# Kernel tuning notes

Hardware: AMD Instinct MI355X
Metric: run time of the kernel (lower is better)

## Reference

```python
import jax, jax.numpy as jnp
import numpy as np

B, T, D_MODEL, N_HEAD = 2, 2048, 1024, 16
HEAD_DIM = D_MODEL // N_HEAD


def setup_inputs() -> dict:
    key = jax.random.key(0)
    ks = jax.random.split(key, 4)
    s = 0.02
    return {
        "x": jax.random.normal(ks[0], (B, T, D_MODEL), dtype=jnp.float32),
        "freqs_cis": jnp.zeros((T, HEAD_DIM // 2), dtype=jnp.float32),  # unused under ALiBi
        "Wq": jax.random.normal(ks[1], (D_MODEL, D_MODEL), dtype=jnp.float32) * s,
        "bq": jnp.zeros((D_MODEL,), dtype=jnp.float32),
        "Wkv": jax.random.normal(ks[2], (2 * D_MODEL, D_MODEL), dtype=jnp.float32) * s,
        "bkv": jnp.zeros((2 * D_MODEL,), dtype=jnp.float32),
        "Wo": jax.random.normal(ks[3], (D_MODEL, D_MODEL), dtype=jnp.float32) * s,
        "bo": jnp.zeros((D_MODEL,), dtype=jnp.float32),
    }


def reference(x, freqs_cis, Wq, bq, Wkv, bkv, Wo, bo):
    Bb, Tt, C = x.shape
    H, Dh = N_HEAD, HEAD_DIM
    # projections (torch Linear: x @ W^T + b)
    q = (x @ Wq.T + bq).reshape(Bb, Tt, H, Dh).transpose(0, 2, 1, 3)      # [B,H,T,Dh]
    kv = (x @ Wkv.T + bkv).reshape(Bb, Tt, 2, H, Dh).transpose(2, 0, 3, 1, 4)
    k, v = kv[0], kv[1]                                                    # [B,H,T,Dh]
    scores = jnp.einsum('bhqd,bhkd->bhqk', q, k) * (1.0 / np.sqrt(Dh))
    # ALiBi: linear slopes (1/H ... 1.0), bias = slope * (j - i)
    slopes = jnp.arange(1, H + 1, dtype=jnp.float32) / H                   # [H]
    pos = jnp.arange(Tt, dtype=jnp.float32)
    dist = pos[None, :] - pos[:, None]                                     # [T,T], j - i
    scores = scores + slopes[:, None, None] * dist[None]                   # broadcast over B
    # causal mask (upper triangle -> -inf)
    causal = pos[:, None] >= pos[None, :]                                  # [T,T] keep-mask
    scores = jnp.where(causal[None, None], scores, -jnp.inf)
    attn = jax.nn.softmax(scores, axis=-1)
    y = jnp.einsum('bhqk,bhkd->bhqd', attn, v)                             # [B,H,T,Dh]
    y = y.transpose(0, 2, 1, 3).reshape(Bb, Tt, C)
    return y @ Wo.T + bo
```

## Files before the change

### kernel.cpp

```cpp
#include <hip/hip_runtime.h>

typedef unsigned short u16;
typedef __bf16 bf16x8 __attribute__((ext_vector_type(8)));
typedef unsigned short u16x8 __attribute__((ext_vector_type(8)));
typedef float f32x4 __attribute__((ext_vector_type(4)));

#define KEY(r) ((((r) ^ ((r) >> 3)) & 7) << 3)

static __device__ __forceinline__ u16 f2b(float f) {
  union { float f; unsigned u; } x; x.f = f;
  unsigned r = x.u + 0x7FFFu + ((x.u >> 16) & 1u);
  return (u16)(r >> 16);
}

static __device__ __forceinline__ bf16x8 ld_frag(const u16* p) {
  union { u16x8 s; bf16x8 b; } u;
  u.s = *reinterpret_cast<const u16x8*>(p);
  return u.b;
}

__global__ __launch_bounds__(256) void cvt_f32_bf16(const float* __restrict__ in,
                                                    u16* __restrict__ out, int n4) {
  int i = blockIdx.x * 256 + threadIdx.x;
  if (i >= n4) return;
  float4 v = reinterpret_cast<const float4*>(in)[i];
  ushort4 o;
  o.x = f2b(v.x); o.y = f2b(v.y); o.z = f2b(v.z); o.w = f2b(v.w);
  reinterpret_cast<ushort4*>(out)[i] = o;
}

template <bool OUT_BF16>
static __device__ __forceinline__ void gemm_body(
    const u16* __restrict__ A, const u16* __restrict__ Bt,
    const float* __restrict__ bias, void* __restrict__ outp,
    int N, int K, int row0, int col0, float scale) {
  __shared__ alignas(16) u16 As[128 * 64];
  __shared__ alignas(16) u16 Bs[128 * 64];
  const int tid = threadIdx.x, wid = tid >> 6, lane = tid & 63;
  const int wr = wid >> 1, wc = wid & 1;
  const int lr = lane >> 3;
  const int lc = (lane & 7) * 8;
  const int frow = lane & 15, fk = (lane >> 4) * 8;
  f32x4 acc[4][4] = {};

  for (int k0 = 0; k0 < K; k0 += 64) {
    __syncthreads();
#pragma unroll
    for (int t = 0; t < 4; ++t) {
      const int r = wid * 32 + t * 8 + lr;
      __builtin_amdgcn_global_load_lds(
          (const __attribute__((address_space(1))) unsigned int*)(
              A + (size_t)(row0 + r) * K + k0 + (lc ^ KEY(r))),
          (__attribute__((address_space(3))) unsigned int*)(As + (wid * 32 + t * 8) * 64),
          16, 0, 0);
    }
#pragma unroll
    for (int t = 0; t < 4; ++t) {
      const int r = wid * 32 + t * 8 + lr;
      __builtin_amdgcn_global_load_lds(
          (const __attribute__((address_space(1))) unsigned int*)(
              Bt + (size_t)(col0 + r) * K + k0 + (lc ^ KEY(r))),
          (__attribute__((address_space(3))) unsigned int*)(Bs + (wid * 32 + t * 8) * 64),
          16, 0, 0);
    }
    __syncthreads();
#pragma unroll
    for (int ks = 0; ks < 2; ++ks) {
      bf16x8 a[4], b[4];
#pragma unroll
      for (int m = 0; m < 4; ++m) {
        const int r = wr * 64 + m * 16 + frow;
        a[m] = ld_frag(&As[r * 64 + ((ks * 32 + fk) ^ KEY(r))]);
      }
#pragma unroll
      for (int n = 0; n < 4; ++n) {
        const int r = wc * 64 + n * 16 + frow;
        b[n] = ld_frag(&Bs[r * 64 + ((ks * 32 + fk) ^ KEY(r))]);
      }
#pragma unroll
      for (int m = 0; m < 4; ++m)
#pragma unroll
        for (int n = 0; n < 4; ++n)
          acc[m][n] = __builtin_amdgcn_mfma_f32_16x16x32_bf16(a[m], b[n], acc[m][n], 0, 0, 0);
    }
  }
  const int colL = lane & 15, rb = (lane >> 4) * 4;
#pragma unroll
  for (int n = 0; n < 4; ++n) {
    const int gc = col0 + wc * 64 + n * 16 + colL;
    const float bv = bias[gc];
#pragma unroll
    for (int m = 0; m < 4; ++m)
#pragma unroll
      for (int r = 0; r < 4; ++r) {
        const int gr = row0 + wr * 64 + m * 16 + rb + r;
        const float v = (acc[m][n][r] + bv) * scale;
        if constexpr (OUT_BF16)
          reinterpret_cast<u16*>(outp)[(size_t)gr * N + gc] = f2b(v);
        else
          reinterpret_cast<float*>(outp)[(size_t)gr * N + gc] = v;
      }
  }
}

__global__ __launch_bounds__(256) void gemm_qkv(
    const u16* __restrict__ xb, const u16* __restrict__ wqb,
    const u16* __restrict__ wkvb, const float* __restrict__ bq,
    const float* __restrict__ bkv, u16* __restrict__ qb, u16* __restrict__ kvb) {
  const int row0 = blockIdx.x * 128;
  const int by = blockIdx.y;
  const u16* Bt; const float* bias; u16* out; int N, col0; float scale;
  if (by < 8) { Bt = wqb;  bias = bq;  out = qb;  N = 1024; col0 = by * 128;      scale = 0.125f; }
  else        { Bt = wkvb; bias = bkv; out = kvb; N = 2048; col0 = (by - 8) * 128; scale = 1.0f; }
  gemm_body<true>(xb, Bt, bias, out, N, 1024, row0, col0, scale);
}

__global__ __launch_bounds__(256) void gemm_o(
    const u16* __restrict__ yb, const u16* __restrict__ wob,
    const float* __restrict__ bo, float* __restrict__ out) {
  gemm_body<false>(yb, wob, bo, out, 1024, 1024, blockIdx.x * 128, blockIdx.y * 128, 1.0f);
}

__global__ __launch_bounds__(128) void attn_kernel(
    const u16* __restrict__ qb,
    const u16* __restrict__ kvb,
    u16* __restrict__ yb,
    int T) {
  const int C = 1024;
  const int bh = blockIdx.x;
  const int qt = gridDim.y - 1 - blockIdx.y;
  const int b = bh >> 4, h = bh & 15;
  const float slope = (float)(h + 1) * 0.0625f;
  const int tid = threadIdx.x, wid = tid >> 6, lane = tid & 63;
  const int qBase = qt * 32;

  __shared__ alignas(16) u16 Ks[64 * 64];
  __shared__ alignas(16) u16 Vt[64 * 64];
  __shared__ alignas(16) u16 Ps[2][16 * 64];

  const int frow = lane & 15, fk = (lane >> 4) * 8;
  const int col = lane & 15, rb = (lane >> 4) * 4;
  const int pk = ((lane >> 4) & 3) << 3;

  const int q_row = qBase + wid * 16 + frow;
  const u16* qp = qb + (size_t)(b * T + q_row) * C + h * 64;
  const bf16x8 aq0 = ld_frag(qp + fk);
  const bf16x8 aq1 = ld_frag(qp + 32 + fk);

  float mrow[4] = {-1e30f, -1e30f, -1e30f, -1e30f};
  float lrow[4] = {0.f, 0.f, 0.f, 0.f};
  f32x4 accO[4] = {};

  const int st_r = tid >> 3;
  const int st_c = (tid & 7) * 8;
  const int vkj = tid & 7;

  const int nt = (qBase + 31) / 64 + 1;

  int4 kreg[4], vreg[4];
#pragma unroll
  for (int t = 0; t < 4; ++t) {
    const int r = st_r + 16 * t;
    const size_t g = (size_t)(b * T + r) * 2048 + h * 64 + st_c;
    kreg[t] = *reinterpret_cast<const int4*>(&kvb[g]);
    vreg[t] = *reinterpret_cast<const int4*>(&kvb[g + 1024]);
  }

  for (int kt = 0; kt < nt; ++kt) {
    const int kBase = kt * 64;
#pragma unroll
    for (int t = 0; t < 4; ++t) {
      const int r = st_r + 16 * t;
      *reinterpret_cast<int4*>(&Ks[r * 64 + (st_c ^ KEY(r))]) = kreg[t];
      const u16* pv = reinterpret_cast<const u16*>(&vreg[t]);
#pragma unroll
      for (int j = 0; j < 8; ++j) {
        const int d = st_c + j;
        Vt[d * 64 + (r ^ ((((j) ^ vkj) & 7) << 3))] = pv[j];
      }
    }
    __syncthreads();
    if (kt + 1 < nt) {
#pragma unroll
      for (int t = 0; t < 4; ++t) {
        const int r = st_r + 16 * t;
        const size_t g = (size_t)(b * T + kBase + 64 + r) * 2048 + h * 64 + st_c;
        kreg[t] = *reinterpret_cast<const int4*>(&kvb[g]);
        vreg[t] = *reinterpret_cast<const int4*>(&kvb[g + 1024]);
      }
    }

    f32x4 accS[4] = {};
    __builtin_amdgcn_s_setprio(1);
#pragma unroll
    for (int n = 0; n < 4; ++n) {
      const int r = n * 16 + frow;
      bf16x8 bk0 = ld_frag(&Ks[r * 64 + (fk ^ KEY(r))]);
      accS[n] = __builtin_amdgcn_mfma_f32_16x16x32_bf16(aq0, bk0, accS[n], 0, 0, 0);
      bf16x8 bk1 = ld_frag(&Ks[r * 64 + ((32 + fk) ^ KEY(r))]);
      accS[n] = __builtin_amdgcn_mfma_f32_16x16x32_bf16(aq1, bk1, accS[n], 0, 0, 0);
    }
    __builtin_amdgcn_s_setprio(0);

    float bn[4]; int kg[4];
#pragma unroll
    for (int n = 0; n < 4; ++n) { kg[n] = kBase + n * 16 + col; bn[n] = slope * (float)kg[n]; }
#pragma unroll
    for (int r = 0; r < 4; ++r) {
      const int qg = qBase + wid * 16 + rb + r;
      float s[4];
      float tmax = -1e30f;
#pragma unroll
      for (int n = 0; n < 4; ++n) {
        float v = accS[n][r] + bn[n];
        if (kg[n] > qg) v = -1e30f;
        s[n] = v;
        tmax = fmaxf(tmax, v);
      }
      tmax = fmaxf(tmax, __shfl_xor(tmax, 1));
      tmax = fmaxf(tmax, __shfl_xor(tmax, 2));
      tmax = fmaxf(tmax, __shfl_xor(tmax, 4));
      tmax = fmaxf(tmax, __shfl_xor(tmax, 8));
      const float newm = fmaxf(mrow[r], tmax);
      const float corr = __expf(mrow[r] - newm);
      mrow[r] = newm;
      float psum = 0.f;
#pragma unroll
      for (int n = 0; n < 4; ++n) {
        const float p = __expf(s[n] - newm);
        psum += p;
        Ps[wid][(rb + r) * 64 + ((n * 16 + col) ^ pk)] = f2b(p);
      }
      psum += __shfl_xor(psum, 1);
      psum += __shfl_xor(psum, 2);
      psum += __shfl_xor(psum, 4);
      psum += __shfl_xor(psum, 8);
      lrow[r] = lrow[r] * corr + psum;
#pragma unroll
      for (int n = 0; n < 4; ++n) accO[n][r] *= corr;
    }

    __builtin_amdgcn_s_setprio(1);
#pragma unroll
    for (int ks = 0; ks < 2; ++ks) {
      const int pkr = ((frow >> 2) & 3) << 3;
      bf16x8 ap = ld_frag(&Ps[wid][frow * 64 + ((ks * 32 + fk) ^ pkr)]);
#pragma unroll
      for (int n = 0; n < 4; ++n) {
        const int d = n * 16 + frow;
        bf16x8 bv = ld_frag(&Vt[d * 64 + ((ks * 32 + fk) ^ KEY(d))]);
        accO[n] = __builtin_amdgcn_mfma_f32_16x16x32_bf16(ap, bv, accO[n], 0, 0, 0);
      }
    }
    __builtin_amdgcn_s_setprio(0);
    __syncthreads();
  }

#pragma unroll
  for (int r = 0; r < 4; ++r) {
    const float inv = 1.0f / lrow[r];
    const int qg = qBase + wid * 16 + rb + r;
    u16* yrow = yb + (size_t)(b * T + qg) * C + h * 64;
#pragma unroll
    for (int n = 0; n < 4; ++n) yrow[n * 16 + col] = f2b(accO[n][r] * inv);
  }
}

extern "C" void kernel_launch(void* const* d_in, const int* in_sizes, int n_in,
                              void* d_out, int out_size, void* d_ws, size_t ws_size,
                              hipStream_t stream) {
  const float* x   = (const float*)d_in[0];
  const float* Wq  = (const float*)d_in[2];
  const float* bq  = (const float*)d_in[3];
  const float* Wkv = (const float*)d_in[4];
  const float* bkv = (const float*)d_in[5];
  const float* Wo  = (const float*)d_in[6];
  const float* bo  = (const float*)d_in[7];
  float* out = (float*)d_out;

  const int B = 2, T = 2048, C = 1024;
  const int M = B * T;

  char* ws = (char*)d_ws;
  u16* xb   = (u16*)(ws + 0);
  u16* wqb  = (u16*)(ws + 8388608);
  u16* wkvb = (u16*)(ws + 10485760);
  u16* wob  = (u16*)(ws + 14680064);
  u16* qb   = (u16*)(ws + 16777216);
  u16* kvb  = (u16*)(ws + 25165824);
  u16* yb   = (u16*)(ws + 41943040);

  cvt_f32_bf16<<<(M * C / 4 + 255) / 256, 256, 0, stream>>>(x, xb, M * C / 4);
  cvt_f32_bf16<<<(C * C / 4 + 255) / 256, 256, 0, stream>>>(Wq, wqb, C * C / 4);
  cvt_f32_bf16<<<(2 * C * C / 4 + 255) / 256, 256, 0, stream>>>(Wkv, wkvb, 2 * C * C / 4);
  cvt_f32_bf16<<<(C * C / 4 + 255) / 256, 256, 0, stream>>>(Wo, wob, C * C / 4);

  gemm_qkv<<<dim3(M / 128, 8 + 16), 256, 0, stream>>>(xb, wqb, wkvb, bq, bkv, qb, kvb);
  attn_kernel<<<dim3(B * 16, T / 32), 128, 0, stream>>>(qb, kvb, yb, T);
  gemm_o<<<dim3(M / 128, C / 128), 256, 0, stream>>>(yb, wob, bo, out);
}
```

Baseline: 259.4 us.

## Enlarge attention query tile to 128 rows and narrow output GEMM tile

The attention kernel now processes 128 query rows per block with 4 waves, each handling two 16-row fragments. Each K/V tile loaded into LDS is therefore reused across four times more queries, which cuts redundant K/V global traffic and staging work. The output projection GEMM is templated on its N tile and uses 64-column tiles, doubling its grid for better occupancy on the CU count. The trade-off is fewer attention blocks, coarser causal granularity (some fully masked tiles get computed), and more registers per wave.

```diff
diff --git a/kernel.cpp b/kernel.cpp
--- a/kernel.cpp
+++ b/kernel.cpp
@@ -29,19 +29,20 @@
   reinterpret_cast<ushort4*>(out)[i] = o;
 }
 
-template <bool OUT_BF16>
+template <bool OUT_BF16, int BN>
 static __device__ __forceinline__ void gemm_body(
     const u16* __restrict__ A, const u16* __restrict__ Bt,
     const float* __restrict__ bias, void* __restrict__ outp,
     int N, int K, int row0, int col0, float scale) {
+  constexpr int NF = BN / 32;
   __shared__ alignas(16) u16 As[128 * 64];
-  __shared__ alignas(16) u16 Bs[128 * 64];
+  __shared__ alignas(16) u16 Bs[BN * 64];
   const int tid = threadIdx.x, wid = tid >> 6, lane = tid & 63;
   const int wr = wid >> 1, wc = wid & 1;
   const int lr = lane >> 3;
   const int lc = (lane & 7) * 8;
   const int frow = lane & 15, fk = (lane >> 4) * 8;
-  f32x4 acc[4][4] = {};
+  f32x4 acc[4][NF] = {};
 
   for (int k0 = 0; k0 < K; k0 += 64) {
     __syncthreads();
@@ -55,39 +56,39 @@
           16, 0, 0);
     }
 #pragma unroll
-    for (int t = 0; t < 4; ++t) {
-      const int r = wid * 32 + t * 8 + lr;
+    for (int t = 0; t < NF; ++t) {
+      const int r = wid * (BN / 4) + t * 8 + lr;
       __builtin_amdgcn_global_load_lds(
           (const __attribute__((address_space(1))) unsigned int*)(
               Bt + (size_t)(col0 + r) * K + k0 + (lc ^ KEY(r))),
-          (__attribute__((address_space(3))) unsigned int*)(Bs + (wid * 32 + t * 8) * 64),
+          (__attribute__((address_space(3))) unsigned int*)(Bs + (wid * (BN / 4) + t * 8) * 64),
           16, 0, 0);
     }
     __syncthreads();
 #pragma unroll
     for (int ks = 0; ks < 2; ++ks) {
-      bf16x8 a[4], b[4];
+      bf16x8 a[4], b[NF];
 #pragma unroll
       for (int m = 0; m < 4; ++m) {
         const int r = wr * 64 + m * 16 + frow;
         a[m] = ld_frag(&As[r * 64 + ((ks * 32 + fk) ^ KEY(r))]);
       }
 #pragma unroll
-      for (int n = 0; n < 4; ++n) {
-        const int r = wc * 64 + n * 16 + frow;
+      for (int n = 0; n < NF; ++n) {
+        const int r = wc * (BN / 2) + n * 16 + frow;
         b[n] = ld_frag(&Bs[r * 64 + ((ks * 32 + fk) ^ KEY(r))]);
       }
 #pragma unroll
       for (int m = 0; m < 4; ++m)
 #pragma unroll
-        for (int n = 0; n < 4; ++n)
+        for (int n = 0; n < NF; ++n)
           acc[m][n] = __builtin_amdgcn_mfma_f32_16x16x32_bf16(a[m], b[n], acc[m][n], 0, 0, 0);
     }
   }
   const int colL = lane & 15, rb = (lane >> 4) * 4;
 #pragma unroll
-  for (int n = 0; n < 4; ++n) {
-    const int gc = col0 + wc * 64 + n * 16 + colL;
+  for (int n = 0; n < NF; ++n) {
+    const int gc = col0 + wc * (BN / 2) + n * 16 + colL;
     const float bv = bias[gc];
 #pragma unroll
     for (int m = 0; m < 4; ++m)
@@ -112,16 +113,16 @@
   const u16* Bt; const float* bias; u16* out; int N, col0; float scale;
   if (by < 8) { Bt = wqb;  bias = bq;  out = qb;  N = 1024; col0 = by * 128;      scale = 0.125f; }
   else        { Bt = wkvb; bias = bkv; out = kvb; N = 2048; col0 = (by - 8) * 128; scale = 1.0f; }
-  gemm_body<true>(xb, Bt, bias, out, N, 1024, row0, col0, scale);
+  gemm_body<true, 128>(xb, Bt, bias, out, N, 1024, row0, col0, scale);
 }
 
 __global__ __launch_bounds__(256) void gemm_o(
     const u16* __restrict__ yb, const u16* __restrict__ wob,
     const float* __restrict__ bo, float* __restrict__ out) {
-  gemm_body<false>(yb, wob, bo, out, 1024, 1024, blockIdx.x * 128, blockIdx.y * 128, 1.0f);
-}
-
-__global__ __launch_bounds__(128) void attn_kernel(
+  gemm_body<false, 64>(yb, wob, bo, out, 1024, 1024, blockIdx.x * 128, blockIdx.y * 64, 1.0f);
+}
+
+__global__ __launch_bounds__(256) void attn_kernel(
     const u16* __restrict__ qb,
     const u16* __restrict__ kvb,
     u16* __restrict__ yb,
@@ -132,35 +133,42 @@
   const int b = bh >> 4, h = bh & 15;
   const float slope = (float)(h + 1) * 0.0625f;
   const int tid = threadIdx.x, wid = tid >> 6, lane = tid & 63;
-  const int qBase = qt * 32;
+  const int qBase = qt * 128;
 
   __shared__ alignas(16) u16 Ks[64 * 64];
   __shared__ alignas(16) u16 Vt[64 * 64];
-  __shared__ alignas(16) u16 Ps[2][16 * 64];
+  __shared__ alignas(16) u16 Ps[4][32 * 64];
 
   const int frow = lane & 15, fk = (lane >> 4) * 8;
   const int col = lane & 15, rb = (lane >> 4) * 4;
   const int pk = ((lane >> 4) & 3) << 3;
 
-  const int q_row = qBase + wid * 16 + frow;
-  const u16* qp = qb + (size_t)(b * T + q_row) * C + h * 64;
-  const bf16x8 aq0 = ld_frag(qp + fk);
-  const bf16x8 aq1 = ld_frag(qp + 32 + fk);
-
-  float mrow[4] = {-1e30f, -1e30f, -1e30f, -1e30f};
-  float lrow[4] = {0.f, 0.f, 0.f, 0.f};
-  f32x4 accO[4] = {};
+  bf16x8 aq[2][2];
+#pragma unroll
+  for (int m = 0; m < 2; ++m) {
+    const int q_row = qBase + wid * 32 + m * 16 + frow;
+    const u16* qp = qb + (size_t)(b * T + q_row) * C + h * 64;
+    aq[m][0] = ld_frag(qp + fk);
+    aq[m][1] = ld_frag(qp + 32 + fk);
+  }
+
+  float mrow[2][4], lrow[2][4];
+  f32x4 accO[2][4] = {};
+#pragma unroll
+  for (int m = 0; m < 2; ++m)
+#pragma unroll
+    for (int r = 0; r < 4; ++r) { mrow[m][r] = -1e30f; lrow[m][r] = 0.f; }
 
   const int st_r = tid >> 3;
   const int st_c = (tid & 7) * 8;
   const int vkj = tid & 7;
 
-  const int nt = (qBase + 31) / 64 + 1;
-
-  int4 kreg[4], vreg[4];
-#pragma unroll
-  for (int t = 0; t < 4; ++t) {
-    const int r = st_r + 16 * t;
+  const int nt = 2 * qt + 2;
+
+  int4 kreg[2], vreg[2];
+#pragma unroll
+  for (int t = 0; t < 2; ++t) {
+    const int r = st_r + 32 * t;
     const size_t g = (size_t)(b * T + r) * 2048 + h * 64 + st_c;
     kreg[t] = *reinterpret_cast<const int4*>(&kvb[g]);
     vreg[t] = *reinterpret_cast<const int4*>(&kvb[g + 1024]);
@@ -169,36 +177,39 @@
   for (int kt = 0; kt < nt; ++kt) {
     const int kBase = kt * 64;
 #pragma unroll
-    for (int t = 0; t < 4; ++t) {
-      const int r = st_r + 16 * t;
+    for (int t = 0; t < 2; ++t) {
+      const int r = st_r + 32 * t;
       *reinterpret_cast<int4*>(&Ks[r * 64 + (st_c ^ KEY(r))]) = kreg[t];
       const u16* pv = reinterpret_cast<const u16*>(&vreg[t]);
 #pragma unroll
       for (int j = 0; j < 8; ++j) {
         const int d = st_c + j;
-        Vt[d * 64 + (r ^ ((((j) ^ vkj) & 7) << 3))] = pv[j];
+        Vt[d * 64 + (r ^ (((j ^ vkj) & 7) << 3))] = pv[j];
       }
     }
     __syncthreads();
     if (kt + 1 < nt) {
 #pragma unroll
-      for (int t = 0; t < 4; ++t) {
-        const int r = st_r + 16 * t;
+      for (int t = 0; t < 2; ++t) {
+        const int r = st_r + 32 * t;
         const size_t g = (size_t)(b * T + kBase + 64 + r) * 2048 + h * 64 + st_c;
         kreg[t] = *reinterpret_cast<const int4*>(&kvb[g]);
         vreg[t] = *reinterpret_cast<const int4*>(&kvb[g + 1024]);
       }
     }
 
-    f32x4 accS[4] = {};
+    f32x4 accS[2][4] = {};
     __builtin_amdgcn_s_setprio(1);
 #pragma unroll
     for (int n = 0; n < 4; ++n) {
       const int r = n * 16 + frow;
       bf16x8 bk0 = ld_frag(&Ks[r * 64 + (fk ^ KEY(r))]);
-      accS[n] = __builtin_amdgcn_mfma_f32_16x16x32_bf16(aq0, bk0, accS[n], 0, 0, 0);
       bf16x8 bk1 = ld_frag(&Ks[r * 64 + ((32 + fk) ^ KEY(r))]);
-      accS[n] = __builtin_amdgcn_mfma_f32_16x16x32_bf16(aq1, bk1, accS[n], 0, 0, 0);
+#pragma unroll
+      for (int m = 0; m < 2; ++m) {
+        accS[m][n] = __builtin_amdgcn_mfma_f32_16x16x32_bf16(aq[m][0], bk0, accS[m][n], 0, 0, 0);
+        accS[m][n] = __builtin_amdgcn_mfma_f32_16x16x32_bf16(aq[m][1], bk1, accS[m][n], 0, 0, 0);
+      }
     }
     __builtin_amdgcn_s_setprio(0);
 
@@ -206,50 +217,57 @@
 #pragma unroll
     for (int n = 0; n < 4; ++n) { kg[n] = kBase + n * 16 + col; bn[n] = slope * (float)kg[n]; }
 #pragma unroll
-    for (int r = 0; r < 4; ++r) {
-      const int qg = qBase + wid * 16 + rb + r;
-      float s[4];
-      float tmax = -1e30f;
-#pragma unroll
-      for (int n = 0; n < 4; ++n) {
-        float v = accS[n][r] + bn[n];
-        if (kg[n] > qg) v = -1e30f;
-        s[n] = v;
-        tmax = fmaxf(tmax, v);
-      }
-      tmax = fmaxf(tmax, __shfl_xor(tmax, 1));
-      tmax = fmaxf(tmax, __shfl_xor(tmax, 2));
-      tmax = fmaxf(tmax, __shfl_xor(tmax, 4));
-      tmax = fmaxf(tmax, __shfl_xor(tmax, 8));
-      const float newm = fmaxf(mrow[r], tmax);
-      const float corr = __expf(mrow[r] - newm);
-      mrow[r] = newm;
-      float psum = 0.f;
-#pragma unroll
-      for (int n = 0; n < 4; ++n) {
-        const float p = __expf(s[n] - newm);
-        psum += p;
-        Ps[wid][(rb + r) * 64 + ((n * 16 + col) ^ pk)] = f2b(p);
-      }
-      psum += __shfl_xor(psum, 1);
-      psum += __shfl_xor(psum, 2);
-      psum += __shfl_xor(psum, 4);
-      psum += __shfl_xor(psum, 8);
-      lrow[r] = lrow[r] * corr + psum;
-#pragma unroll
-      for (int n = 0; n < 4; ++n) accO[n][r] *= corr;
-    }
+    for (int m = 0; m < 2; ++m)
+#pragma unroll
+      for (int r = 0; r < 4; ++r) {
+        const int qg = qBase + wid * 32 + m * 16 + rb + r;
+        float s[4];
+        float tmax = -1e30f;
+#pragma unroll
+        for (int n = 0; n < 4; ++n) {
+          float v = accS[m][n][r] + bn[n];
+          if (kg[n] > qg) v = -1e30f;
+          s[n] = v;
+          tmax = fmaxf(tmax, v);
+        }
+        tmax = fmaxf(tmax, __shfl_xor(tmax, 1));
+        tmax = fmaxf(tmax, __shfl_xor(tmax, 2));
+        tmax = fmaxf(tmax, __shfl_xor(tmax, 4));
+        tmax = fmaxf(tmax, __shfl_xor(tmax, 8));
+        const float newm = fmaxf(mrow[m][r], tmax);
+        const float corr = __expf(mrow[m][r] - newm);
+        mrow[m][r] = newm;
+        float psum = 0.f;
+#pragma unroll
+        for (int n = 0; n < 4; ++n) {
+          const float p = __expf(s[n] - newm);
+          psum += p;
+          Ps[wid][(m * 16 + rb + r) * 64 + ((n * 16 + col) ^ pk)] = f2b(p);
+        }
+        psum += __shfl_xor(psum, 1);
+        psum += __shfl_xor(psum, 2);
+        psum += __shfl_xor(psum, 4);
+        psum += __shfl_xor(psum, 8);
+        lrow[m][r] = lrow[m][r] * corr + psum;
+#pragma unroll
+        for (int n = 0; n < 4; ++n) accO[m][n][r] *= corr;
+      }
 
     __builtin_amdgcn_s_setprio(1);
 #pragma unroll
     for (int ks = 0; ks < 2; ++ks) {
       const int pkr = ((frow >> 2) & 3) << 3;
-      bf16x8 ap = ld_frag(&Ps[wid][frow * 64 + ((ks * 32 + fk) ^ pkr)]);
+      bf16x8 ap[2];
+#pragma unroll
+      for (int m = 0; m < 2; ++m)
+        ap[m] = ld_frag(&Ps[wid][(m * 16 + frow) * 64 + ((ks * 32 + fk) ^ pkr)]);
 #pragma unroll
       for (int n = 0; n < 4; ++n) {
         const int d = n * 16 + frow;
         bf16x8 bv = ld_frag(&Vt[d * 64 + ((ks * 32 + fk) ^ KEY(d))]);
-        accO[n] = __builtin_amdgcn_mfma_f32_16x16x32_bf16(ap, bv, accO[n], 0, 0, 0);
+#pragma unroll
+        for (int m = 0; m < 2; ++m)
+          accO[m][n] = __builtin_amdgcn_mfma_f32_16x16x32_bf16(ap[m], bv, accO[m][n], 0, 0, 0);
       }
     }
     __builtin_amdgcn_s_setprio(0);
@@ -257,13 +275,15 @@
   }
 
 #pragma unroll
-  for (int r = 0; r < 4; ++r) {
-    const float inv = 1.0f / lrow[r];
-    const int qg = qBase + wid * 16 + rb + r;
-    u16* yrow = yb + (size_t)(b * T + qg) * C + h * 64;
-#pragma unroll
-    for (int n = 0; n < 4; ++n) yrow[n * 16 + col] = f2b(accO[n][r] * inv);
-  }
+  for (int m = 0; m < 2; ++m)
+#pragma unroll
+    for (int r = 0; r < 4; ++r) {
+      const float inv = 1.0f / lrow[m][r];
+      const int qg = qBase + wid * 32 + m * 16 + rb + r;
+      u16* yrow = yb + (size_t)(b * T + qg) * C + h * 64;
+#pragma unroll
+      for (int n = 0; n < 4; ++n) yrow[n * 16 + col] = f2b(accO[m][n][r] * inv);
+    }
 }
 
 extern "C" void kernel_launch(void* const* d_in, const int* in_sizes, int n_in,
@@ -296,6 +316,6 @@
   cvt_f32_bf16<<<(C * C / 4 + 255) / 256, 256, 0, stream>>>(Wo, wob, C * C / 4);
 
   gemm_qkv<<<dim3(M / 128, 8 + 16), 256, 0, stream>>>(xb, wqb, wkvb, bq, bkv, qb, kvb);
-  attn_kernel<<<dim3(B * 16, T / 32), 128, 0, stream>>>(qb, kvb, yb, T);
-  gemm_o<<<dim3(M / 128, C / 128), 256, 0, stream>>>(yb, wob, bo, out);
-}
+  attn_kernel<<<dim3(B * 16, T / 128), 256, 0, stream>>>(qb, kvb, yb, T);
+  gemm_o<<<dim3(M / 128, C / 64), 256, 0, stream>>>(yb, wob, bo, out);
+}
```

After: 262.5 us. About the same (+1.2%).
